# Kernel tuning notes

Hardware: AMD Instinct MI355X
Metric: run time of the kernel (lower is better)

The kernel has to match this reference:

```python
import jax, jax.numpy as jnp
import numpy as np
import math

D_MODEL = 1024
D_STATE = 128
D_CONV = 4
D_INNER = 2048  # expand * d_model
DT_RANK = 64    # ceil(d_model / 16)
DT_MIN = 1e-3
DT_MAX = 0.1
BATCH = 2
SEQ = 2048


def setup_inputs() -> dict:
    key = jax.random.key(0)
    ks = jax.random.split(key, 8)
    x = jax.random.normal(ks[0], (BATCH, SEQ, D_MODEL), jnp.float32)
    W_in = jax.random.normal(ks[1], (2 * D_INNER, D_MODEL), jnp.float32) / math.sqrt(D_MODEL)
    W_out = jax.random.normal(ks[2], (D_MODEL, D_INNER), jnp.float32) / math.sqrt(D_INNER)
    conv_w = jax.random.normal(ks[3], (D_INNER, 1, D_CONV), jnp.float32) / math.sqrt(D_CONV)
    conv_b = jnp.zeros((D_INNER,), jnp.float32)
    W_x = jax.random.normal(ks[4], (DT_RANK + 2 * D_STATE, D_INNER), jnp.float32) / math.sqrt(D_INNER)
    dt_std = DT_RANK ** (-0.5) * DT_MAX
    W_dt = jax.random.uniform(ks[5], (D_INNER, DT_RANK), jnp.float32, -dt_std, dt_std)
    dt = jnp.exp(jax.random.uniform(ks[6], (D_INNER,), jnp.float32)
                 * (math.log(DT_MAX) - math.log(DT_MIN)) + math.log(DT_MIN))
    dt = jnp.clip(dt, DT_MIN, None)
    b_dt = dt + jnp.log(-jnp.expm1(-dt))  # inverse softplus init
    A_log = jnp.log(jnp.tile(jnp.arange(1, D_STATE + 1, dtype=jnp.float32), (D_INNER, 1)))
    Dp = jnp.ones((D_INNER,), jnp.float32)
    return {"x": x, "W_in": W_in, "W_out": W_out, "conv_w": conv_w, "conv_b": conv_b,
            "W_x": W_x, "W_dt": W_dt, "b_dt": b_dt, "A_log": A_log, "Dp": Dp}


def _silu(v):
    return v * jax.nn.sigmoid(v)


def _forward(x, W_in, W_out, conv_w, conv_b, W_x, W_dt, b_dt, A_log, Dp):
    bsz, seqlen, _ = x.shape
    xz = x @ W_in.T                              # (B, L, 2*D_INNER)
    xc, z = jnp.split(xz, 2, axis=-1)
    # causal depthwise conv1d (torch pads d_conv-1 both sides then truncates to L)
    xc_t = xc.transpose(0, 2, 1)                 # (B, D_INNER, L)
    conv = jax.lax.conv_general_dilated(
        xc_t, conv_w, window_strides=(1,), padding=[(D_CONV - 1, 0)],
        feature_group_count=D_INNER, dimension_numbers=('NCH', 'OIH', 'NCH'))
    u = _silu((conv + conv_b[None, :, None]).transpose(0, 2, 1))  # (B, L, D_INNER)

    # selective scan
    x_dbl = u @ W_x.T                            # (B, L, DT_RANK + 2*D_STATE)
    dt_lo = x_dbl[..., :DT_RANK]
    Bm = x_dbl[..., DT_RANK:DT_RANK + D_STATE]   # (B, L, N)
    Cm = x_dbl[..., DT_RANK + D_STATE:]          # (B, L, N)
    # NOTE: faithful to original, which adds dt_proj.bias twice
    dt = jax.nn.softplus(dt_lo @ W_dt.T + 2.0 * b_dt)  # (B, L, D_INNER)
    A = -jnp.exp(A_log)                          # (D_INNER, N)

    def step(h, inp):
        dt_t, B_t, C_t, u_t = inp                # (B,D),(B,N),(B,N),(B,D)
        dA = jnp.exp(dt_t[:, :, None] * A[None])            # (B, D, N)
        h = dA * h + (dt_t * u_t)[:, :, None] * B_t[:, None, :]
        y = jnp.einsum('bdn,bn->bd', h, C_t)
        return h, y

    h0 = jnp.zeros((bsz, D_INNER, D_STATE), u.dtype)
    _, ys = jax.lax.scan(step, h0, (dt.transpose(1, 0, 2), Bm.transpose(1, 0, 2),
                                    Cm.transpose(1, 0, 2), u.transpose(1, 0, 2)))
    y = ys.transpose(1, 0, 2) + u * Dp           # (B, L, D_INNER)
    y = y * _silu(z)
    return y @ W_out.T                           # (B, L, D_MODEL)


def reference(x, W_in, W_out, conv_w, conv_b, W_x, W_dt, b_dt, A_log, Dp):
    return _forward(x, W_in, W_out, conv_w, conv_b, W_x, W_dt, b_dt, A_log, Dp)
```

## Files before the change

### kernel.cpp

```cpp
#include <hip/hip_runtime.h>
#include <stdint.h>
#include <math.h>

#define D_MODEL 1024
#define D_STATE 128
#define D_INNER 2048
#define DT_RANK 64
#define BATCH   2
#define SEQ     2048
#define TOKENS  (BATCH*SEQ)
#define NPROJ   (DT_RANK + 2*D_STATE)

typedef unsigned short u16;
typedef __attribute__((ext_vector_type(4))) float f32x4;
typedef __attribute__((ext_vector_type(8))) short s16x8;
typedef __attribute__((ext_vector_type(4))) unsigned short u16x4;

#if __has_builtin(__builtin_amdgcn_exp2f)
#define EXP2(x) __builtin_amdgcn_exp2f(x)
#else
#define EXP2(x) __expf((x) * 0.6931471805599453f)
#endif
#define L2E 1.44269504088896f

static __device__ __forceinline__ u16 f2bf(float f) {
  unsigned u = __builtin_bit_cast(unsigned, f);
  return (u16)((u + 0x7FFFu + ((u >> 16) & 1u)) >> 16);
}
static __device__ __forceinline__ float bf2f(u16 h) {
  return __builtin_bit_cast(float, ((unsigned)h) << 16);
}

static __device__ __forceinline__ void gload_lds16(const void* g, void* l) {
  __builtin_amdgcn_global_load_lds(
      (const __attribute__((address_space(1))) void*)g,
      (__attribute__((address_space(3))) void*)l, 16, 0, 0);
}

__global__ void k_cvt_bf16(const float* __restrict__ in, u16* __restrict__ out, int n4) {
  int i = blockIdx.x * blockDim.x + threadIdx.x;
  if (i >= n4) return;
  f32x4 v = ((const f32x4*)in)[i];
  u16x4 o;
  o.x = f2bf(v.x); o.y = f2bf(v.y); o.z = f2bf(v.z); o.w = f2bf(v.w);
  ((u16x4*)out)[i] = o;
}

#define BM 128
#define BN 128
#define BK 64

template<int EPI>
__global__ __launch_bounds__(256) void k_gemm_bt(
    const u16* __restrict__ A, const u16* __restrict__ B,
    void* __restrict__ C, const float* __restrict__ bias,
    const u16* __restrict__ U,
    int M, int N, int K, int ldc)
{
  __shared__ __align__(16) u16 As[BM*BK];
  __shared__ __align__(16) u16 Bs[BN*BK];
  const int tid  = threadIdx.x;
  const int lane = tid & 63;
  const int wid  = tid >> 6;
  const int wr   = (wid >> 1) * 64;
  const int wc   = (wid & 1) * 64;
  const int bm   = blockIdx.x * BM;
  const int bn   = blockIdx.y * BN;
  const int lr   = lane & 15;
  const int lk   = (lane >> 4) * 8;

  f32x4 acc[4][4] = {};

  for (int k0 = 0; k0 < K; k0 += BK) {
    #pragma unroll
    for (int i = 0; i < 4; ++i) {
      int c   = tid + i * 256;
      int row = c >> 3;
      int col = (c & 7) * 8;
      const u16* ga = A + (size_t)(bm + row) * K + (k0 + col);
      gload_lds16(ga, As + (size_t)c * 8);
      int brow = bn + row; brow = brow < N ? brow : N - 1;
      const u16* gb = B + (size_t)brow * K + (k0 + col);
      gload_lds16(gb, Bs + (size_t)c * 8);
    }
    __syncthreads();

    #pragma unroll
    for (int kk = 0; kk < BK; kk += 32) {
      s16x8 af[4], bf[4];
      #pragma unroll
      for (int m = 0; m < 4; ++m)
        af[m] = *(const s16x8*)(As + (size_t)(wr + m*16 + lr) * BK + kk + lk);
      #pragma unroll
      for (int n = 0; n < 4; ++n)
        bf[n] = *(const s16x8*)(Bs + (size_t)(wc + n*16 + lr) * BK + kk + lk);
      #pragma unroll
      for (int m = 0; m < 4; ++m)
        #pragma unroll
        for (int n = 0; n < 4; ++n)
          acc[m][n] = __builtin_amdgcn_mfma_f32_16x16x32_bf16(af[m], bf[n], acc[m][n], 0, 0, 0);
    }
    __syncthreads();
  }

  const int orow0 = bm + wr + (lane >> 4) * 4;
  const int ocol0 = bn + wc + lr;
  #pragma unroll
  for (int m = 0; m < 4; ++m) {
    #pragma unroll
    for (int n = 0; n < 4; ++n) {
      int col = ocol0 + n * 16;
      if (col >= N) continue;
      #pragma unroll
      for (int r = 0; r < 4; ++r) {
        int row = orow0 + m * 16 + r;
        float v = acc[m][n][r];
        if (EPI == 3) {
          v = v + 2.0f * bias[col];
          v = (v > 20.0f) ? v : log1pf(__expf(v));
          float uu = bf2f(U[(size_t)row * D_INNER + col]);
          ((float2*)C)[(size_t)col * TOKENS + row] = make_float2(v * L2E, v * uu);
        } else if (EPI == 1) {
          ((u16*)C)[(size_t)row * ldc + col] = f2bf(v);
        } else {
          ((float*)C)[(size_t)row * ldc + col] = v;
        }
      }
    }
  }
}

__global__ __launch_bounds__(256) void k_conv_silu(
    const u16* __restrict__ xz, const float* __restrict__ cw,
    const float* __restrict__ cb, u16* __restrict__ u)
{
  int idx = blockIdx.x * 256 + threadIdx.x;
  int d   = idx & (D_INNER - 1);
  int tok = idx >> 11;
  int t   = tok & (SEQ - 1);
  int b   = tok >> 11;
  f32x4 w = *(const f32x4*)(cw + (size_t)d * 4);
  float acc = cb[d];
  #pragma unroll
  for (int j = 0; j < 4; ++j) {
    int tt = t - 3 + j;
    if (tt >= 0)
      acc += bf2f(xz[(size_t)(b * SEQ + tt) * (2*D_INNER) + d]) * w[j];
  }
  float s = acc / (1.0f + __expf(-acc));
  u[(size_t)tok * D_INNER + d] = f2bf(s);
}

__global__ void k_split(const float* __restrict__ xdbl, u16* __restrict__ dtlo,
                        float* __restrict__ BC)
{
  int idx = blockIdx.x * 256 + threadIdx.x;
  if (idx >= TOKENS * NPROJ) return;
  int row = idx / NPROJ;
  int c   = idx - row * NPROJ;
  float v = xdbl[idx];
  if (c < DT_RANK) {
    dtlo[(size_t)row * DT_RANK + c] = f2bf(v);
  } else if (c < DT_RANK + D_STATE) {
    int n = c - DT_RANK;
    BC[(size_t)row * 256 + (n >> 1) * 4 + (n & 1)] = v;
  } else {
    int n = c - DT_RANK - D_STATE;
    BC[(size_t)row * 256 + (n >> 1) * 4 + 2 + (n & 1)] = v;
  }
}

#define SCHUNK 32
#define RPAD 65

__global__ __launch_bounds__(256, 4) void k_scan(
    const float2* __restrict__ dtq, const float* __restrict__ BC,
    const float* __restrict__ A_log, u16* __restrict__ ysT)
{
  __shared__ float red[4][SCHUNK * RPAD];
  const int lane = threadIdx.x & 63;
  const int wid  = threadIdx.x >> 6;
  const int gw = blockIdx.x * 4 + wid;
  const int b = gw >> 11;
  const int d = gw & (D_INNER - 1);

  float2 al = *(const float2*)(A_log + (size_t)d * D_STATE + 2 * lane);
  const float A0 = -__expf(al.x);
  const float A1 = -__expf(al.y);
  float h0 = 0.f, h1 = 0.f;

  const float2* dbase = dtq + (size_t)d * TOKENS + b * SEQ;
  asm("" : "+v"(dbase));
  const float* BCb = BC + (size_t)b * SEQ * 256 + 4 * lane;
  u16* yo = ysT + ((size_t)d * BATCH + b) * SEQ;

  float* myred = red[wid];
  const int r  = lane & 31;
  const int hf = lane >> 5;
  const float* rrow = myred + r * RPAD + hf * 32;

  for (int t0 = 0; t0 < SEQ; t0 += SCHUNK) {
    #pragma unroll
    for (int tt = 0; tt < SCHUNK; ++tt) {
      float2 sd = dbase[t0 + tt];
      f32x4 bc = *(const f32x4*)(BCb + (size_t)(t0 + tt) * 256);
      float dA0 = EXP2(sd.x * A0);
      float dA1 = EXP2(sd.x * A1);
      h0 = fmaf(dA0, h0, sd.y * bc.x);
      h1 = fmaf(dA1, h1, sd.y * bc.y);
      float yp = fmaf(h1, bc.w, h0 * bc.z);
      myred[tt * RPAD + lane] = yp;
    }
    float s0 = 0.f, s1 = 0.f, s2 = 0.f, s3 = 0.f;
    #pragma unroll
    for (int k = 0; k < 8; ++k) {
      s0 += rrow[k];
      s1 += rrow[k + 8];
      s2 += rrow[k + 16];
      s3 += rrow[k + 24];
    }
    float s = (s0 + s1) + (s2 + s3);
    float y = s + __shfl_xor(s, 32);
    if (hf == 0) yo[t0 + r] = f2bf(y);
  }
}

__global__ __launch_bounds__(256) void k_gate(
    const u16* __restrict__ ysT, const u16* __restrict__ ub,
    const u16* __restrict__ xz, const float* __restrict__ Dp,
    u16* __restrict__ yg)
{
  __shared__ u16 tile[64][68];
  const int tid  = threadIdx.x;
  const int c    = tid & 63;
  const int rb   = tid >> 6;
  const int tok0 = blockIdx.x * 64;
  const int d0   = blockIdx.y * 64;
  const int bb   = tok0 >> 11;
  const int t0   = tok0 & (SEQ - 1);

  #pragma unroll
  for (int j = 0; j < 16; ++j) {
    int dl = rb + j * 4;
    tile[dl][c] = ysT[((size_t)(d0 + dl) * BATCH + bb) * SEQ + t0 + c];
  }
  __syncthreads();
  #pragma unroll
  for (int j = 0; j < 16; ++j) {
    int tl  = rb + j * 4;
    int tok = tok0 + tl;
    int dd  = d0 + c;
    float y = bf2f(tile[c][tl]);
    float uu = bf2f(ub[(size_t)tok * D_INNER + dd]);
    float z  = bf2f(xz[(size_t)tok * (2*D_INNER) + D_INNER + dd]);
    float v  = (y + uu * Dp[dd]) * (z / (1.0f + __expf(-z)));
    yg[(size_t)tok * D_INNER + dd] = f2bf(v);
  }
}

extern "C" void kernel_launch(void* const* d_in, const int* in_sizes, int n_in,
                              void* d_out, int out_size, void* d_ws, size_t ws_size,
                              hipStream_t stream) {
  (void)in_sizes; (void)n_in; (void)out_size; (void)ws_size;
  const float* x      = (const float*)d_in[0];
  const float* W_in   = (const float*)d_in[1];
  const float* W_out  = (const float*)d_in[2];
  const float* conv_w = (const float*)d_in[3];
  const float* conv_b = (const float*)d_in[4];
  const float* W_x    = (const float*)d_in[5];
  const float* W_dt   = (const float*)d_in[6];
  const float* b_dt   = (const float*)d_in[7];
  const float* A_log  = (const float*)d_in[8];
  const float* Dp     = (const float*)d_in[9];

  size_t off = 0;
  char* wsb = (char*)d_ws;
  auto alloc = [&](size_t bytes) -> void* {
    void* p = wsb + off;
    off += (bytes + 255) & ~(size_t)255;
    return p;
  };
  u16*    x_bf    = (u16*)alloc((size_t)TOKENS * D_MODEL * 2);
  u16*    Win_bf  = (u16*)alloc((size_t)2 * D_INNER * D_MODEL * 2);
  u16*    Wx_bf   = (u16*)alloc((size_t)NPROJ * D_INNER * 2);
  u16*    Wdt_bf  = (u16*)alloc((size_t)D_INNER * DT_RANK * 2);
  u16*    Wout_bf = (u16*)alloc((size_t)D_MODEL * D_INNER * 2);
  u16*    xz_bf   = (u16*)alloc((size_t)TOKENS * 2 * D_INNER * 2);
  u16*    u_bf    = (u16*)alloc((size_t)TOKENS * D_INNER * 2);
  float*  xdbl    = (float*)alloc((size_t)TOKENS * NPROJ * 4);
  u16*    dtlo_bf = (u16*)alloc((size_t)TOKENS * DT_RANK * 2);
  float*  BC_f    = (float*)alloc((size_t)TOKENS * 256 * 4);
  float2* dtq     = (float2*)alloc((size_t)TOKENS * D_INNER * 8);
  u16*    ysT     = (u16*)alloc((size_t)D_INNER * TOKENS * 2);
  u16*    yg      = (u16*)alloc((size_t)TOKENS * D_INNER * 2);

  auto cvt = [&](const float* src, u16* dst, size_t n) {
    int n4 = (int)(n / 4);
    k_cvt_bf16<<<(n4 + 255) / 256, 256, 0, stream>>>(src, dst, n4);
  };
  cvt(x,     x_bf,    (size_t)TOKENS * D_MODEL);
  cvt(W_in,  Win_bf,  (size_t)2 * D_INNER * D_MODEL);
  cvt(W_x,   Wx_bf,   (size_t)NPROJ * D_INNER);
  cvt(W_dt,  Wdt_bf,  (size_t)D_INNER * DT_RANK);
  cvt(W_out, Wout_bf, (size_t)D_MODEL * D_INNER);

  dim3 blk(256);
  k_gemm_bt<1><<<dim3(TOKENS/128, (2*D_INNER)/128), blk, 0, stream>>>(
      x_bf, Win_bf, xz_bf, nullptr, nullptr, TOKENS, 2*D_INNER, D_MODEL, 2*D_INNER);
  k_conv_silu<<<(TOKENS * D_INNER) / 256, blk, 0, stream>>>(xz_bf, conv_w, conv_b, u_bf);
  k_gemm_bt<0><<<dim3(TOKENS/128, (NPROJ + 127)/128), blk, 0, stream>>>(
      u_bf, Wx_bf, xdbl, nullptr, nullptr, TOKENS, NPROJ, D_INNER, NPROJ);
  k_split<<<((TOKENS * NPROJ) + 255) / 256, blk, 0, stream>>>(xdbl, dtlo_bf, BC_f);
  k_gemm_bt<3><<<dim3(TOKENS/128, D_INNER/128), blk, 0, stream>>>(
      dtlo_bf, Wdt_bf, dtq, b_dt, u_bf, TOKENS, D_INNER, DT_RANK, 0);
  k_scan<<<(BATCH * D_INNER) / 4, blk, 0, stream>>>(dtq, BC_f, A_log, ysT);
  k_gate<<<dim3(TOKENS/64, D_INNER/64), blk, 0, stream>>>(ysT, u_bf, xz_bf, Dp, yg);
  k_gemm_bt<0><<<dim3(TOKENS/128, D_MODEL/128), blk, 0, stream>>>(
      yg, Wout_bf, d_out, nullptr, nullptr, TOKENS, D_MODEL, D_INNER, D_MODEL);
}
```

Baseline: 618.8 us.

## Split selective scan into sequence segments with head pass and stitch

Replaces the single sequential scan per (batch, channel) with a three-phase chunked scan. A head kernel computes the local end state and the summed dt of each segment, a stitch kernel propagates carry states across segments, and the main kernel rescans each segment from its carried-in state while producing outputs. This exposes up to 16x more independent waves so the whole GPU is used despite the long serial dependence, at the cost of reading dt and B/C roughly twice plus extra workspace traffic. It also shrinks the output reduction chunk to 16 timesteps and loads two timesteps of dt per vector load.

```diff
diff --git a/kernel.cpp b/kernel.cpp
--- a/kernel.cpp
+++ b/kernel.cpp
@@ -10,6 +10,7 @@
 #define SEQ     2048
 #define TOKENS  (BATCH*SEQ)
 #define NPROJ   (DT_RANK + 2*D_STATE)
+#define NCOL    (BATCH*D_INNER)
 
 typedef unsigned short u16;
 typedef __attribute__((ext_vector_type(4))) float f32x4;
@@ -170,58 +171,137 @@
   }
 }
 
-#define SCHUNK 32
+
+__global__ __launch_bounds__(256, 4) void k_scan_head(
+    const float2* __restrict__ dtq, const float* __restrict__ BC,
+    const float* __restrict__ A_log, float* __restrict__ H,
+    float* __restrict__ S, int nseg, int SL)
+{
+  const int lane = threadIdx.x & 63;
+  const int wid  = threadIdx.x >> 6;
+  const unsigned gw = blockIdx.x * 4 + wid;
+  const unsigned nsm1 = nseg - 1;
+  const int col = gw / nsm1;
+  const int s   = gw - col * nsm1;
+  const int b = col >> 11;
+  const int d = col & (D_INNER - 1);
+
+  float2 al = *(const float2*)(A_log + (size_t)d * D_STATE + 2 * lane);
+  const float A0 = -__expf(al.x);
+  const float A1 = -__expf(al.y);
+  float h0 = 0.f, h1 = 0.f, sum = 0.f;
+
+  const f32x4* dptr = (const f32x4*)(dtq + (size_t)d * TOKENS + b * SEQ + s * SL);
+  const float* BCb  = BC + ((size_t)b * SEQ + s * SL) * 256 + 4 * lane;
+
+  for (int c0 = 0; c0 < SL; c0 += 16) {
+    #pragma unroll
+    for (int t2 = 0; t2 < 8; ++t2) {
+      f32x4 sd = dptr[(c0 >> 1) + t2];
+      int tt = c0 + 2 * t2;
+      f32x4 bc = *(const f32x4*)(BCb + (size_t)tt * 256);
+      sum += sd.x;
+      float dA0 = EXP2(sd.x * A0);
+      float dA1 = EXP2(sd.x * A1);
+      h0 = fmaf(dA0, h0, sd.y * bc.x);
+      h1 = fmaf(dA1, h1, sd.y * bc.y);
+      bc = *(const f32x4*)(BCb + (size_t)(tt + 1) * 256);
+      sum += sd.z;
+      dA0 = EXP2(sd.z * A0);
+      dA1 = EXP2(sd.z * A1);
+      h0 = fmaf(dA0, h0, sd.w * bc.x);
+      h1 = fmaf(dA1, h1, sd.w * bc.y);
+    }
+  }
+  *(float2*)(H + ((size_t)col * nseg + s) * D_STATE + 2 * lane) = make_float2(h0, h1);
+  if (lane == 0) S[(size_t)col * nseg + s] = sum;
+}
+
+__global__ __launch_bounds__(256) void k_stitch(
+    const float* __restrict__ A_log, float* __restrict__ H,
+    const float* __restrict__ S, int nseg)
+{
+  const int lane = threadIdx.x & 63;
+  const int wid  = threadIdx.x >> 6;
+  const int col  = blockIdx.x * 4 + wid;
+  const int d = col & (D_INNER - 1);
+
+  float2 al = *(const float2*)(A_log + (size_t)d * D_STATE + 2 * lane);
+  const float A0 = -__expf(al.x);
+  const float A1 = -__expf(al.y);
+  float hin0 = 0.f, hin1 = 0.f;
+
+  for (int s = 0; s < nseg - 1; ++s) {
+    float2* hp = (float2*)(H + ((size_t)col * nseg + s) * D_STATE + 2 * lane);
+    float2 he = *hp;
+    float sm = S[(size_t)col * nseg + s];
+    float d0 = EXP2(A0 * sm);
+    float d1 = EXP2(A1 * sm);
+    hin0 = fmaf(d0, hin0, he.x);
+    hin1 = fmaf(d1, hin1, he.y);
+    *hp = make_float2(hin0, hin1);
+  }
+}
+
+#define SCHUNK 16
 #define RPAD 65
 
-__global__ __launch_bounds__(256, 4) void k_scan(
+__global__ __launch_bounds__(256, 4) void k_scan_main(
     const float2* __restrict__ dtq, const float* __restrict__ BC,
-    const float* __restrict__ A_log, u16* __restrict__ ysT)
+    const float* __restrict__ A_log, const float* __restrict__ H,
+    u16* __restrict__ ysT, int nseg, int lognseg, int SL)
 {
   __shared__ float red[4][SCHUNK * RPAD];
   const int lane = threadIdx.x & 63;
   const int wid  = threadIdx.x >> 6;
-  const int gw = blockIdx.x * 4 + wid;
-  const int b = gw >> 11;
-  const int d = gw & (D_INNER - 1);
+  const unsigned gw = blockIdx.x * 4 + wid;
+  const int seg = gw & (nseg - 1);
+  const int col = gw >> lognseg;
+  const int b = col >> 11;
+  const int d = col & (D_INNER - 1);
 
   float2 al = *(const float2*)(A_log + (size_t)d * D_STATE + 2 * lane);
   const float A0 = -__expf(al.x);
   const float A1 = -__expf(al.y);
   float h0 = 0.f, h1 = 0.f;
-
-  const float2* dbase = dtq + (size_t)d * TOKENS + b * SEQ;
-  asm("" : "+v"(dbase));
-  const float* BCb = BC + (size_t)b * SEQ * 256 + 4 * lane;
-  u16* yo = ysT + ((size_t)d * BATCH + b) * SEQ;
+  if (seg > 0) {
+    float2 hv = *(const float2*)(H + ((size_t)col * nseg + seg - 1) * D_STATE + 2 * lane);
+    h0 = hv.x; h1 = hv.y;
+  }
+
+  const f32x4* dptr = (const f32x4*)(dtq + (size_t)d * TOKENS + b * SEQ + seg * SL);
+  const float* BCb  = BC + ((size_t)b * SEQ + seg * SL) * 256 + 4 * lane;
+  u16* yo = ysT + ((size_t)d * BATCH + b) * SEQ + seg * SL;
 
   float* myred = red[wid];
-  const int r  = lane & 31;
-  const int hf = lane >> 5;
-  const float* rrow = myred + r * RPAD + hf * 32;
-
-  for (int t0 = 0; t0 < SEQ; t0 += SCHUNK) {
-    #pragma unroll
-    for (int tt = 0; tt < SCHUNK; ++tt) {
-      float2 sd = dbase[t0 + tt];
-      f32x4 bc = *(const f32x4*)(BCb + (size_t)(t0 + tt) * 256);
+  const int r = lane & 15;
+  const int q = lane >> 4;
+  const float* rrow = myred + r * RPAD + q * 16;
+
+  for (int c0 = 0; c0 < SL; c0 += SCHUNK) {
+    #pragma unroll
+    for (int t2 = 0; t2 < 8; ++t2) {
+      f32x4 sd = dptr[(c0 >> 1) + t2];
+      int tt = 2 * t2;
+      f32x4 bc = *(const f32x4*)(BCb + (size_t)(c0 + tt) * 256);
       float dA0 = EXP2(sd.x * A0);
       float dA1 = EXP2(sd.x * A1);
       h0 = fmaf(dA0, h0, sd.y * bc.x);
       h1 = fmaf(dA1, h1, sd.y * bc.y);
-      float yp = fmaf(h1, bc.w, h0 * bc.z);
-      myred[tt * RPAD + lane] = yp;
+      myred[tt * RPAD + lane] = fmaf(h1, bc.w, h0 * bc.z);
+      bc = *(const f32x4*)(BCb + (size_t)(c0 + tt + 1) * 256);
+      dA0 = EXP2(sd.z * A0);
+      dA1 = EXP2(sd.z * A1);
+      h0 = fmaf(dA0, h0, sd.w * bc.x);
+      h1 = fmaf(dA1, h1, sd.w * bc.y);
+      myred[(tt + 1) * RPAD + lane] = fmaf(h1, bc.w, h0 * bc.z);
     }
-    float s0 = 0.f, s1 = 0.f, s2 = 0.f, s3 = 0.f;
-    #pragma unroll
-    for (int k = 0; k < 8; ++k) {
-      s0 += rrow[k];
-      s1 += rrow[k + 8];
-      s2 += rrow[k + 16];
-      s3 += rrow[k + 24];
-    }
-    float s = (s0 + s1) + (s2 + s3);
-    float y = s + __shfl_xor(s, 32);
-    if (hf == 0) yo[t0 + r] = f2bf(y);
+    float s0 = 0.f;
+    #pragma unroll
+    for (int k = 0; k < 16; ++k) s0 += rrow[k];
+    s0 += __shfl_xor(s0, 16);
+    s0 += __shfl_xor(s0, 32);
+    if (lane < 16) yo[c0 + r] = f2bf(s0);
   }
 }
 
@@ -261,7 +341,7 @@
 extern "C" void kernel_launch(void* const* d_in, const int* in_sizes, int n_in,
                               void* d_out, int out_size, void* d_ws, size_t ws_size,
                               hipStream_t stream) {
-  (void)in_sizes; (void)n_in; (void)out_size; (void)ws_size;
+  (void)in_sizes; (void)n_in; (void)out_size;
   const float* x      = (const float*)d_in[0];
   const float* W_in   = (const float*)d_in[1];
   const float* W_out  = (const float*)d_in[2];
@@ -294,6 +374,15 @@
   u16*    ysT     = (u16*)alloc((size_t)D_INNER * TOKENS * 2);
   u16*    yg      = (u16*)alloc((size_t)TOKENS * D_INNER * 2);
 
+  int nseg = 1, lognseg = 0;
+  for (int cand = 16, lg = 4; cand > 1; cand >>= 1, --lg) {
+    size_t need = ((size_t)NCOL * cand * D_STATE * 4 + 255 + (size_t)NCOL * cand * 4 + 255);
+    if (off + need <= ws_size) { nseg = cand; lognseg = lg; break; }
+  }
+  float* Hbuf = (float*)alloc((size_t)NCOL * nseg * D_STATE * 4);
+  float* Sbuf = (float*)alloc((size_t)NCOL * nseg * 4);
+  const int SL = SEQ / nseg;
+
   auto cvt = [&](const float* src, u16* dst, size_t n) {
     int n4 = (int)(n / 4);
     k_cvt_bf16<<<(n4 + 255) / 256, 256, 0, stream>>>(src, dst, n4);
@@ -313,7 +402,13 @@
   k_split<<<((TOKENS * NPROJ) + 255) / 256, blk, 0, stream>>>(xdbl, dtlo_bf, BC_f);
   k_gemm_bt<3><<<dim3(TOKENS/128, D_INNER/128), blk, 0, stream>>>(
       dtlo_bf, Wdt_bf, dtq, b_dt, u_bf, TOKENS, D_INNER, DT_RANK, 0);
-  k_scan<<<(BATCH * D_INNER) / 4, blk, 0, stream>>>(dtq, BC_f, A_log, ysT);
+  if (nseg > 1) {
+    k_scan_head<<<(NCOL * (nseg - 1)) / 4, blk, 0, stream>>>(
+        dtq, BC_f, A_log, Hbuf, Sbuf, nseg, SL);
+    k_stitch<<<NCOL / 4, blk, 0, stream>>>(A_log, Hbuf, Sbuf, nseg);
+  }
+  k_scan_main<<<(NCOL * nseg) / 4, blk, 0, stream>>>(
+      dtq, BC_f, A_log, Hbuf, ysT, nseg, lognseg, SL);
   k_gate<<<dim3(TOKENS/64, D_INNER/64), blk, 0, stream>>>(ysT, u_bf, xz_bf, Dp, yg);
   k_gemm_bt<0><<<dim3(TOKENS/128, D_MODEL/128), blk, 0, stream>>>(
       yg, Wout_bf, d_out, nullptr, nullptr, TOKENS, D_MODEL, D_INNER, D_MODEL);
```

After: 970.8 us. +56.9%, slower.
